# Optimization experiments

Hardware: AMD Instinct MI355X
Metric: run time of the kernel (lower is better)

Reference implementation:

```python
import jax, jax.numpy as jnp
import numpy as np

FILTERS = 256
KH, KW = 3, 3
SH, SW = 1, 1
IN_CH = 128


def setup_inputs() -> dict:
    key = jax.random.key(0)
    k1, k2 = jax.random.split(key)
    inputs = jax.random.normal(k1, (32, 112, 112, IN_CH), dtype=jnp.float32)
    # Glorot-uniform init matching the layer's build()
    limit = np.sqrt(6.0 / (KH * KW * IN_CH + FILTERS)).astype(np.float32)
    kernel = jax.random.uniform(k2, (KH, KW, IN_CH, FILTERS), dtype=jnp.float32,
                                minval=-limit, maxval=limit)
    bias = jnp.zeros((FILTERS,), dtype=jnp.float32)
    return {"inputs": inputs, "kernel": kernel, "bias": bias}


def reference(inputs, kernel, bias):
    # Equivalent math to extract_patches(SAME) + flattened matmul + bias:
    # a standard 2D convolution in NHWC with HWIO kernel.
    out = jax.lax.conv_general_dilated(
        inputs, kernel,
        window_strides=(SH, SW),
        padding="SAME",
        dimension_numbers=("NHWC", "HWIO", "NHWC"),
    )
    return out + bias
```

## Files before the change

### kernel.cpp

```cpp
#include <hip/hip_runtime.h>

typedef __attribute__((ext_vector_type(4)))  float   floatx4;
typedef __attribute__((ext_vector_type(16))) float   floatx16;
typedef __attribute__((ext_vector_type(8)))  __bf16  bf16x8;
typedef unsigned short ushort_t;
typedef __attribute__((ext_vector_type(8)))  ushort_t ushortx8;

typedef const unsigned int __attribute__((address_space(1)))* gptr_t;
typedef unsigned int __attribute__((address_space(3)))* lptr_t;

#define NIMG 32
#define H    112
#define W    112
#define CIN  128
#define COUT 256
#define HP   114
#define WP   114
#define HW   12544

#define BM 128
#define BN 128
#define NT 18
#define NBLK 6272

#define PREPAD_BLOCKS 12996
#define WTRANS_BLOCKS 1152

__device__ __forceinline__ ushort_t f32_to_bf16(float f) {
    unsigned u = __float_as_uint(f);
    unsigned r = 0x7fffu + ((u >> 16) & 1u);
    return (ushort_t)((u + r) >> 16);
}

__global__ __launch_bounds__(256) void prepass_fused(const float* __restrict__ in,
                                                     const float* __restrict__ k,
                                                     ushort_t* __restrict__ pad,
                                                     ushort_t* __restrict__ wt) {
    int bid = blockIdx.x;
    if (bid < PREPAD_BLOCKS) {
        int u    = bid * 256 + threadIdx.x;
        int ic16 = u & 7;
        int sp   = u >> 3;
        int iw   = sp % WP;
        int sp2  = sp / WP;
        int ih   = sp2 % HP;
        int n    = sp2 / HP;
        ushortx8 v0, v1;
        if (ih >= 1 && ih <= H && iw >= 1 && iw <= W) {
            const float* src = in + ((size_t)((n * H + (ih - 1)) * W + (iw - 1))) * CIN + ic16 * 16;
            floatx4 a = *reinterpret_cast<const floatx4*>(src);
            floatx4 b = *reinterpret_cast<const floatx4*>(src + 4);
            floatx4 c = *reinterpret_cast<const floatx4*>(src + 8);
            floatx4 d = *reinterpret_cast<const floatx4*>(src + 12);
#pragma unroll
            for (int j = 0; j < 4; ++j) {
                v0[j] = f32_to_bf16(a[j]); v0[4 + j] = f32_to_bf16(b[j]);
                v1[j] = f32_to_bf16(c[j]); v1[4 + j] = f32_to_bf16(d[j]);
            }
        } else {
#pragma unroll
            for (int j = 0; j < 8; ++j) { v0[j] = 0; v1[j] = 0; }
        }
        ushortx8* dst = reinterpret_cast<ushortx8*>(pad) + ((size_t)sp * 16 + ic16 * 2);
        dst[0] = v0;
        dst[1] = v1;
    } else {
        int t    = (bid - PREPAD_BLOCKS) * 256 + threadIdx.x;
        int ic   = t & 127;
        int oc   = (t >> 7) & 255;
        int khkw = t >> 15;
        wt[t] = f32_to_bf16(k[((size_t)(khkw * CIN + ic)) * COUT + oc]);
    }
}

__device__ __forceinline__ int aoffK(int t) {
    int tap = t >> 1;
    return ((tap / 3) * WP + (tap % 3)) * CIN + (t & 1) * 64;
}
__device__ __forceinline__ int boffK(int t) {
    int tap = t >> 1;
    return tap * (COUT * CIN) + (t & 1) * 64;
}


__global__ __launch_bounds__(256, 3) void conv_mfma4(const ushort_t* __restrict__ pad,
                                                     const ushort_t* __restrict__ wt,
                                                     const float* __restrict__ bias,
                                                     float* __restrict__ out) {
    __shared__ __align__(16) ushort_t lds[24576];

    const int tid  = threadIdx.x;
    const int wid  = tid >> 6;
    const int lane = tid & 63;
    const int wm   = wid >> 1;
    const int wn   = wid & 1;
    const int bid  = blockIdx.x;
    const int swz  = (bid & 7) * (NBLK / 8) + (bid >> 3);
    const int mi   = swz >> 1;
    const int ni   = swz & 1;

    const int trow = tid >> 3;
    const int lc   = (tid & 7) ^ (trow & 7) ^ ((trow >> 3) & 3);

    const ushort_t* srcA[4];
    const ushort_t* srcB[4];
#pragma unroll
    for (int s = 0; s < 4; ++s) {
        int m  = mi * BM + s * 32 + trow;
        int n  = m / HW;
        int r  = m % HW;
        int oh = r / W;
        int ow = r % W;
        srcA[s] = pad + ((size_t)((n * HP + oh) * WP + ow)) * CIN + lc * 8;
        srcB[s] = wt + (size_t)(ni * BN + s * 32 + trow) * CIN + lc * 8;
    }
    const int dstSlot = wid * 512;

#define STAGE_A(par, s_, oA)                                                                        \
    __builtin_amdgcn_global_load_lds((gptr_t)(srcA[s_] + (oA)),                                     \
                                     (lptr_t)&lds[(par) * 8192 + (s_) * 2048 + dstSlot], 16, 0, 0);
#define STAGE_B(s_, oB)                                                                             \
    __builtin_amdgcn_global_load_lds((gptr_t)(srcB[s_] + (oB)),                                     \
                                     (lptr_t)&lds[16384 + (s_) * 2048 + dstSlot], 16, 0, 0);

    const int aBase = (wm * 64 + (lane & 31)) * 64;
    const int bBase = 16384 + (wn * 64 + (lane & 31)) * 64;
    const int gr    = (lane & 7) ^ ((lane >> 3) & 3);
    int cOff[4];
#pragma unroll
    for (int ksl = 0; ksl < 4; ++ksl)
        cOff[ksl] = ((ksl * 2 + (lane >> 5)) ^ gr) * 8;

    floatx16 acc[2][2];
#pragma unroll
    for (int i = 0; i < 2; ++i)
#pragma unroll
        for (int j = 0; j < 2; ++j) acc[i][j] = (floatx16)0.0f;

    {
        const int oA0 = aoffK(0);
        const int oB0 = boffK(0);
        STAGE_A(0, 0, oA0); STAGE_A(0, 1, oA0); STAGE_A(0, 2, oA0); STAGE_A(0, 3, oA0);
        STAGE_B(0, oB0); STAGE_B(1, oB0); STAGE_B(2, oB0); STAGE_B(3, oB0);
    }
    asm volatile("s_waitcnt vmcnt(0)" ::: "memory");
    __builtin_amdgcn_s_barrier();

    for (int t = 0; t < NT; ++t) {
        const int par  = t & 1;
        const int parn = par ^ 1;
        const int oAn  = aoffK(t + 1);
        const int oBn  = boffK(t + 1);
        const int aB   = par * 8192 + aBase;
        bf16x8 af[4], bfr0[4], bfr1[4];

#pragma unroll
        for (int ksl = 0; ksl < 4; ++ksl) {
            af[ksl]   = *reinterpret_cast<const bf16x8*>(&lds[aB + cOff[ksl]]);
            bfr0[ksl] = *reinterpret_cast<const bf16x8*>(&lds[bBase + cOff[ksl]]);
        }
        if (t + 1 < NT) { STAGE_A(parn, 0, oAn); STAGE_A(parn, 2, oAn); }
        __builtin_amdgcn_s_setprio(1);
#pragma unroll
        for (int ksl = 0; ksl < 4; ++ksl)
            acc[0][0] = __builtin_amdgcn_mfma_f32_32x32x16_bf16(af[ksl], bfr0[ksl], acc[0][0], 0, 0, 0);
#pragma unroll
        for (int ksl = 0; ksl < 4; ++ksl)
            bfr1[ksl] = *reinterpret_cast<const bf16x8*>(&lds[bBase + 2048 + cOff[ksl]]);
#pragma unroll
        for (int ksl = 0; ksl < 4; ++ksl)
            acc[0][1] = __builtin_amdgcn_mfma_f32_32x32x16_bf16(af[ksl], bfr1[ksl], acc[0][1], 0, 0, 0);
        __builtin_amdgcn_s_setprio(0);
        if (t + 1 < NT) { asm volatile("s_waitcnt vmcnt(2)" ::: "memory"); }
        else            { asm volatile("s_waitcnt vmcnt(0)" ::: "memory"); }
        __builtin_amdgcn_s_barrier();

#pragma unroll
        for (int ksl = 0; ksl < 4; ++ksl)
            af[ksl] = *reinterpret_cast<const bf16x8*>(&lds[aB + 2048 + cOff[ksl]]);
        if (t + 1 < NT) {
            STAGE_B(0, oBn); STAGE_B(1, oBn); STAGE_B(2, oBn); STAGE_B(3, oBn);
            STAGE_A(parn, 1, oAn); STAGE_A(parn, 3, oAn);
        }
        __builtin_amdgcn_s_setprio(1);
#pragma unroll
        for (int ksl = 0; ksl < 4; ++ksl) {
            acc[1][0] = __builtin_amdgcn_mfma_f32_32x32x16_bf16(af[ksl], bfr0[ksl], acc[1][0], 0, 0, 0);
            acc[1][1] = __builtin_amdgcn_mfma_f32_32x32x16_bf16(af[ksl], bfr1[ksl], acc[1][1], 0, 0, 0);
        }
        __builtin_amdgcn_s_setprio(0);
        if (t + 1 < NT) { asm volatile("s_waitcnt vmcnt(2)" ::: "memory"); }
        __builtin_amdgcn_s_barrier();
    }

    const int colL = ni * BN + wn * 64 + (lane & 31);
    const int rowL = mi * BM + wm * 64 + 4 * (lane >> 5);
    float bv[2];
#pragma unroll
    for (int cb = 0; cb < 2; ++cb) bv[cb] = bias[colL + cb * 32];
#pragma unroll
    for (int rf = 0; rf < 2; ++rf)
#pragma unroll
        for (int cb = 0; cb < 2; ++cb)
#pragma unroll
            for (int reg = 0; reg < 16; ++reg) {
                int row = rowL + rf * 32 + (reg & 3) + 8 * (reg >> 2);
                out[(size_t)row * COUT + colL + cb * 32] = acc[rf][cb][reg] + bv[cb];
            }
#undef STAGE_A
#undef STAGE_B
}

extern "C" void kernel_launch(void* const* d_in, const int* in_sizes, int n_in,
                              void* d_out, int out_size, void* d_ws, size_t ws_size,
                              hipStream_t stream) {
    const float* input = (const float*)d_in[0];
    const float* kern  = (const float*)d_in[1];
    const float* bias  = (const float*)d_in[2];
    float* out         = (float*)d_out;

    ushort_t* pad = (ushort_t*)d_ws;
    ushort_t* wt  = pad + (size_t)NIMG * HP * WP * CIN;

    prepass_fused<<<PREPAD_BLOCKS + WTRANS_BLOCKS, 256, 0, stream>>>(input, kern, pad, wt);
    conv_mfma4<<<NBLK, 256, 0, stream>>>(pad, wt, bias, out);
}
```

Before: 342.8 us.

## Enlarge conv GEMM M tile to 256 rows with 4x2 MFMA accumulators per wave

Doubles the block tile along M from 128 to 256 output pixels, so each wave now computes a 128x64 sub-tile with eight 32x32 accumulators. This halves the grid and reuses each loaded weight tile across twice as many rows. The aim is less global/LDS traffic per MFMA and a higher compute-to-load ratio. In exchange, LDS per block and register pressure go up, occupancy drops (launch bounds go from 3 to 2), and the pipeline now waits for all loads (vmcnt(0)) instead of keeping two in flight.

```diff
diff --git a/kernel.cpp b/kernel.cpp
--- a/kernel.cpp
+++ b/kernel.cpp
@@ -18,10 +18,10 @@
 #define WP   114
 #define HW   12544
 
-#define BM 128
+#define BM 256
 #define BN 128
 #define NT 18
-#define NBLK 6272
+#define NBLK 3136
 
 #define PREPAD_BLOCKS 12996
 #define WTRANS_BLOCKS 1152
@@ -83,11 +83,11 @@
 }
 
 
-__global__ __launch_bounds__(256, 3) void conv_mfma4(const ushort_t* __restrict__ pad,
+__global__ __launch_bounds__(256, 2) void conv_mfma4(const ushort_t* __restrict__ pad,
                                                      const ushort_t* __restrict__ wt,
                                                      const float* __restrict__ bias,
                                                      float* __restrict__ out) {
-    __shared__ __align__(16) ushort_t lds[24576];
+    __shared__ __align__(16) ushort_t lds[40960];
 
     const int tid  = threadIdx.x;
     const int wid  = tid >> 6;
@@ -102,46 +102,51 @@
     const int trow = tid >> 3;
     const int lc   = (tid & 7) ^ (trow & 7) ^ ((trow >> 3) & 3);
 
-    const ushort_t* srcA[4];
-    const ushort_t* srcB[4];
-#pragma unroll
-    for (int s = 0; s < 4; ++s) {
+    int offA[8];
+#pragma unroll
+    for (int s = 0; s < 8; ++s) {
         int m  = mi * BM + s * 32 + trow;
         int n  = m / HW;
         int r  = m % HW;
         int oh = r / W;
         int ow = r % W;
-        srcA[s] = pad + ((size_t)((n * HP + oh) * WP + ow)) * CIN + lc * 8;
-        srcB[s] = wt + (size_t)(ni * BN + s * 32 + trow) * CIN + lc * 8;
-    }
+        offA[s] = ((n * HP + oh) * WP + ow) * CIN + lc * 8;
+    }
+    int offB[4];
+#pragma unroll
+    for (int s = 0; s < 4; ++s)
+        offB[s] = (ni * BN + s * 32 + trow) * CIN + lc * 8;
+
     const int dstSlot = wid * 512;
 
 #define STAGE_A(par, s_, oA)                                                                        \
-    __builtin_amdgcn_global_load_lds((gptr_t)(srcA[s_] + (oA)),                                     \
-                                     (lptr_t)&lds[(par) * 8192 + (s_) * 2048 + dstSlot], 16, 0, 0);
+    __builtin_amdgcn_global_load_lds((gptr_t)(pad + offA[s_] + (oA)),                               \
+                                     (lptr_t)&lds[(par) * 16384 + (s_) * 2048 + dstSlot], 16, 0, 0);
 #define STAGE_B(s_, oB)                                                                             \
-    __builtin_amdgcn_global_load_lds((gptr_t)(srcB[s_] + (oB)),                                     \
-                                     (lptr_t)&lds[16384 + (s_) * 2048 + dstSlot], 16, 0, 0);
-
-    const int aBase = (wm * 64 + (lane & 31)) * 64;
-    const int bBase = 16384 + (wn * 64 + (lane & 31)) * 64;
+    __builtin_amdgcn_global_load_lds((gptr_t)(wt + offB[s_] + (oB)),                                \
+                                     (lptr_t)&lds[32768 + (s_) * 2048 + dstSlot], 16, 0, 0);
+
+    const int aBase = (wm * 4) * 2048 + (lane & 31) * 64;
+    const int bBase = 32768 + (wn * 2) * 2048 + (lane & 31) * 64;
     const int gr    = (lane & 7) ^ ((lane >> 3) & 3);
     int cOff[4];
 #pragma unroll
     for (int ksl = 0; ksl < 4; ++ksl)
         cOff[ksl] = ((ksl * 2 + (lane >> 5)) ^ gr) * 8;
 
-    floatx16 acc[2][2];
-#pragma unroll
-    for (int i = 0; i < 2; ++i)
+    floatx16 acc[4][2];
+#pragma unroll
+    for (int i = 0; i < 4; ++i)
 #pragma unroll
         for (int j = 0; j < 2; ++j) acc[i][j] = (floatx16)0.0f;
 
     {
         const int oA0 = aoffK(0);
         const int oB0 = boffK(0);
-        STAGE_A(0, 0, oA0); STAGE_A(0, 1, oA0); STAGE_A(0, 2, oA0); STAGE_A(0, 3, oA0);
-        STAGE_B(0, oB0); STAGE_B(1, oB0); STAGE_B(2, oB0); STAGE_B(3, oB0);
+#pragma unroll
+        for (int s = 0; s < 8; ++s) STAGE_A(0, s, oA0);
+#pragma unroll
+        for (int s = 0; s < 4; ++s) STAGE_B(s, oB0);
     }
     asm volatile("s_waitcnt vmcnt(0)" ::: "memory");
     __builtin_amdgcn_s_barrier();
@@ -151,61 +156,68 @@
         const int parn = par ^ 1;
         const int oAn  = aoffK(t + 1);
         const int oBn  = boffK(t + 1);
-        const int aB   = par * 8192 + aBase;
-        bf16x8 af[4], bfr0[4], bfr1[4];
-
-#pragma unroll
-        for (int ksl = 0; ksl < 4; ++ksl) {
-            af[ksl]   = *reinterpret_cast<const bf16x8*>(&lds[aB + cOff[ksl]]);
-            bfr0[ksl] = *reinterpret_cast<const bf16x8*>(&lds[bBase + cOff[ksl]]);
-        }
-        if (t + 1 < NT) { STAGE_A(parn, 0, oAn); STAGE_A(parn, 2, oAn); }
+        const int aB   = par * 16384 + aBase;
+        bf16x8 af0[4], af1[4], b0[4], b1[4];
+
+#pragma unroll
+        for (int ksl = 0; ksl < 4; ++ksl) {
+            af0[ksl] = *reinterpret_cast<const bf16x8*>(&lds[aB +        cOff[ksl]]);
+            af1[ksl] = *reinterpret_cast<const bf16x8*>(&lds[aB + 2048 + cOff[ksl]]);
+            b0[ksl]  = *reinterpret_cast<const bf16x8*>(&lds[bBase +     cOff[ksl]]);
+        }
+        if (t + 1 < NT) { STAGE_A(parn, 0, oAn); STAGE_A(parn, 1, oAn); STAGE_A(parn, 2, oAn); STAGE_A(parn, 3, oAn); }
         __builtin_amdgcn_s_setprio(1);
 #pragma unroll
+        for (int ksl = 0; ksl < 4; ++ksl) {
+            acc[0][0] = __builtin_amdgcn_mfma_f32_32x32x16_bf16(af0[ksl], b0[ksl], acc[0][0], 0, 0, 0);
+            acc[1][0] = __builtin_amdgcn_mfma_f32_32x32x16_bf16(af1[ksl], b0[ksl], acc[1][0], 0, 0, 0);
+        }
+#pragma unroll
         for (int ksl = 0; ksl < 4; ++ksl)
-            acc[0][0] = __builtin_amdgcn_mfma_f32_32x32x16_bf16(af[ksl], bfr0[ksl], acc[0][0], 0, 0, 0);
-#pragma unroll
-        for (int ksl = 0; ksl < 4; ++ksl)
-            bfr1[ksl] = *reinterpret_cast<const bf16x8*>(&lds[bBase + 2048 + cOff[ksl]]);
-#pragma unroll
-        for (int ksl = 0; ksl < 4; ++ksl)
-            acc[0][1] = __builtin_amdgcn_mfma_f32_32x32x16_bf16(af[ksl], bfr1[ksl], acc[0][1], 0, 0, 0);
+            b1[ksl] = *reinterpret_cast<const bf16x8*>(&lds[bBase + 2048 + cOff[ksl]]);
+#pragma unroll
+        for (int ksl = 0; ksl < 4; ++ksl) {
+            acc[0][1] = __builtin_amdgcn_mfma_f32_32x32x16_bf16(af0[ksl], b1[ksl], acc[0][1], 0, 0, 0);
+            acc[1][1] = __builtin_amdgcn_mfma_f32_32x32x16_bf16(af1[ksl], b1[ksl], acc[1][1], 0, 0, 0);
+        }
         __builtin_amdgcn_s_setprio(0);
-        if (t + 1 < NT) { asm volatile("s_waitcnt vmcnt(2)" ::: "memory"); }
-        else            { asm volatile("s_waitcnt vmcnt(0)" ::: "memory"); }
         __builtin_amdgcn_s_barrier();
 
 #pragma unroll
-        for (int ksl = 0; ksl < 4; ++ksl)
-            af[ksl] = *reinterpret_cast<const bf16x8*>(&lds[aB + 2048 + cOff[ksl]]);
+        for (int ksl = 0; ksl < 4; ++ksl) {
+            af0[ksl] = *reinterpret_cast<const bf16x8*>(&lds[aB + 4096 + cOff[ksl]]);
+            af1[ksl] = *reinterpret_cast<const bf16x8*>(&lds[aB + 6144 + cOff[ksl]]);
+        }
         if (t + 1 < NT) {
+            STAGE_A(parn, 4, oAn); STAGE_A(parn, 5, oAn); STAGE_A(parn, 6, oAn); STAGE_A(parn, 7, oAn);
             STAGE_B(0, oBn); STAGE_B(1, oBn); STAGE_B(2, oBn); STAGE_B(3, oBn);
-            STAGE_A(parn, 1, oAn); STAGE_A(parn, 3, oAn);
         }
         __builtin_amdgcn_s_setprio(1);
 #pragma unroll
         for (int ksl = 0; ksl < 4; ++ksl) {
-            acc[1][0] = __builtin_amdgcn_mfma_f32_32x32x16_bf16(af[ksl], bfr0[ksl], acc[1][0], 0, 0, 0);
-            acc[1][1] = __builtin_amdgcn_mfma_f32_32x32x16_bf16(af[ksl], bfr1[ksl], acc[1][1], 0, 0, 0);
+            acc[2][0] = __builtin_amdgcn_mfma_f32_32x32x16_bf16(af0[ksl], b0[ksl], acc[2][0], 0, 0, 0);
+            acc[3][0] = __builtin_amdgcn_mfma_f32_32x32x16_bf16(af1[ksl], b0[ksl], acc[3][0], 0, 0, 0);
+            acc[2][1] = __builtin_amdgcn_mfma_f32_32x32x16_bf16(af0[ksl], b1[ksl], acc[2][1], 0, 0, 0);
+            acc[3][1] = __builtin_amdgcn_mfma_f32_32x32x16_bf16(af1[ksl], b1[ksl], acc[3][1], 0, 0, 0);
         }
         __builtin_amdgcn_s_setprio(0);
-        if (t + 1 < NT) { asm volatile("s_waitcnt vmcnt(2)" ::: "memory"); }
+        if (t + 1 < NT) { asm volatile("s_waitcnt vmcnt(0)" ::: "memory"); }
         __builtin_amdgcn_s_barrier();
     }
 
-    const int colL = ni * BN + wn * 64 + (lane & 31);
-    const int rowL = mi * BM + wm * 64 + 4 * (lane >> 5);
+    const int colB = ni * BN + wn * 64 + (lane & 31);
+    const int rowB = mi * BM + wm * 128 + 4 * (lane >> 5);
     float bv[2];
 #pragma unroll
-    for (int cb = 0; cb < 2; ++cb) bv[cb] = bias[colL + cb * 32];
-#pragma unroll
-    for (int rf = 0; rf < 2; ++rf)
+    for (int cb = 0; cb < 2; ++cb) bv[cb] = bias[colB + cb * 32];
+#pragma unroll
+    for (int rblk = 0; rblk < 4; ++rblk)
 #pragma unroll
         for (int cb = 0; cb < 2; ++cb)
 #pragma unroll
             for (int reg = 0; reg < 16; ++reg) {
-                int row = rowL + rf * 32 + (reg & 3) + 8 * (reg >> 2);
-                out[(size_t)row * COUT + colL + cb * 32] = acc[rf][cb][reg] + bv[cb];
+                int row = rowB + rblk * 32 + (reg & 3) + 8 * (reg >> 2);
+                out[(size_t)row * COUT + colB + cb * 32] = acc[rblk][cb][reg] + bv[cb];
             }
 #undef STAGE_A
 #undef STAGE_B
```

Result: no change. 348.3 us (+1.6%).
